# Optimization experiments

Measured on AMD Instinct MI355X. Metric: run time of the kernel, lower is better.

The kernel has to match this reference:

```python
import jax, jax.numpy as jnp
import numpy as np

B, T, C, H = 8, 2048, 1024, 128


def setup_inputs() -> dict:
    key = jax.random.key(0)
    k1, k2, k3, k4 = jax.random.split(key, 4)
    x = jax.random.normal(k1, (B, T, C), dtype=jnp.float32)
    # torch nn.Linear(n_embed, head_size, bias=False) weights, stored as [C, H] for x @ W
    scale = 1.0 / np.sqrt(C)
    Wk = jax.random.normal(k2, (C, H), dtype=jnp.float32) * scale
    Wq = jax.random.normal(k3, (C, H), dtype=jnp.float32) * scale
    Wv = jax.random.normal(k4, (C, H), dtype=jnp.float32) * scale
    return {"x": x, "Wk": Wk, "Wq": Wq, "Wv": Wv}


def reference(x, Wk, Wq, Wv):
    # Faithful translation of Head.forward (dropout = identity in eval mode).
    Bx, Tx, Cx = x.shape
    k = x @ Wk  # [B,T,H]
    q = x @ Wq  # [B,T,H]
    v = x @ Wv  # [B,T,H]
    # NOTE: original scales by C**-0.5 (n_embed), not head_size**-0.5.
    scores = jnp.einsum('bth,bsh->bts', q, k) * (Cx ** -0.5)  # [B,T,T]
    causal = jnp.tril(jnp.ones((Tx, Tx), dtype=bool))  # tril buffer
    scores = jnp.where(causal, scores, -jnp.inf)
    weights = jax.nn.softmax(scores, axis=-1)
    out = jnp.einsum('bts,bsh->bth', weights, v)  # [B,T,H]
    return out
```

## Files before the change

kernel.cpp:

```cpp
#include <hip/hip_runtime.h>
#include <type_traits>

#define Bn 8
#define Tn 2048
#define Cn 1024
#define Hn 128
#define Mn (Bn*Tn)

typedef __attribute__((ext_vector_type(4))) float f32x4;
typedef __attribute__((ext_vector_type(2))) float f32x2;
typedef __attribute__((ext_vector_type(16))) float f32x16;
typedef __attribute__((ext_vector_type(8))) short s16x8;
typedef __attribute__((ext_vector_type(4))) int i32x4;
typedef __attribute__((ext_vector_type(2))) int i32x2;
typedef unsigned int u32;

__device__ __forceinline__ unsigned short f2bf(float f) {
  union { float f; unsigned u; } v; v.f = f;
  unsigned r = v.u + 0x7FFFu + ((v.u >> 16) & 1u);
  return (unsigned short)(r >> 16);
}

__device__ __forceinline__ float bf2f(unsigned s) {
  return __builtin_bit_cast(float, s << 16);
}

__device__ __forceinline__ unsigned cvtpk(float lo, float hi) {
  unsigned r;
  asm("v_cvt_pk_bf16_f32 %0, %1, %2" : "=v"(r) : "v"(lo), "v"(hi));
  return r;
}

__device__ __forceinline__ i32x2 swap32(int a, int b) {
#if __has_builtin(__builtin_amdgcn_permlane32_swap)
  return __builtin_amdgcn_permlane32_swap(a, b, false, false);
#else
  int ax = __shfl_xor(a, 32), bx = __shfl_xor(b, 32);
  i32x2 r;
  r[0] = (threadIdx.x & 32) ? bx : a;
  r[1] = (threadIdx.x & 32) ? b : ax;
  return r;
#endif
}

__device__ __forceinline__ void gl_lds16(const void* g, void* l) {
  __builtin_amdgcn_global_load_lds((const __attribute__((address_space(1))) u32*)g,
                                   (__attribute__((address_space(3))) u32*)l, 16, 0, 0);
}

__global__ __launch_bounds__(256) void prep_wt(const float* __restrict__ Wq,
                                               const float* __restrict__ Wk,
                                               const float* __restrict__ Wv,
                                               unsigned short* __restrict__ Wt) {
  __shared__ float tile[64][33];
  const int w = blockIdx.z;
  const float* W = (w == 0) ? Wq : (w == 1) ? Wk : Wv;
  const float scale = (w == 0) ? 0.03125f : 1.0f;
  const int c0 = blockIdx.x * 64, h0 = blockIdx.y * 32;
  const int tid = threadIdx.x;
  const int hl = tid & 31, cg = tid >> 5;
#pragma unroll
  for (int i = 0; i < 8; i++) {
    int cl = cg * 8 + i;
    tile[cl][hl] = W[(c0 + cl) * Hn + h0 + hl];
  }
  __syncthreads();
  const int cl2 = tid & 63, hg = tid >> 6;
#pragma unroll
  for (int i = 0; i < 8; i++) {
    int hl2 = hg * 8 + i;
    Wt[(size_t)(w * Hn + h0 + hl2) * Cn + c0 + cl2] = f2bf(tile[cl2][hl2] * scale);
  }
}

__global__ __launch_bounds__(512, 1) void proj_fused(const float* __restrict__ x,
                                                     const unsigned short* __restrict__ Wt,
                                                     unsigned short* __restrict__ qkv) {
  __shared__ __align__(16) unsigned short Abuf[2][64 * 64];
  __shared__ __align__(16) unsigned short Bbuf[2][384 * 64];
  const int tid = threadIdx.x;
  const int lane = tid & 63, wv = tid >> 6;
  const int wm = wv >> 2, wn = wv & 3;
  const int l31 = lane & 31, hi = lane >> 5;
  const int bm = blockIdx.x * 64;
  const int phase = (blockIdx.x >> 3) & 15;

  const int ar = tid >> 3;
  const int as = tid & 7;

  f32x16 acc[3];
#pragma unroll
  for (int i = 0; i < 3; i++)
#pragma unroll
    for (int r = 0; r < 16; r++) acc[i][r] = 0.f;

  auto slice = [&](int u) { return ((u + phase) & 15) * 64; };

  auto stageB = [&](int buf, int kk) {
#pragma unroll
    for (int i = 0; i < 6; i++) {
      int r0 = wv * 48 + i * 8;
      int n = r0 + (lane >> 3);
      const unsigned short* src = Wt + (size_t)n * Cn + kk + (((lane & 7) ^ (n & 7)) << 3);
      gl_lds16(src, &Bbuf[buf][r0 * 64]);
    }
  };
  auto loadA = [&](int kk, float4& v0, float4& v1) {
    const float* g = x + (size_t)(bm + ar) * Cn + kk + as * 8;
    v0 = *(const float4*)g;
    v1 = *(const float4*)(g + 4);
  };
  auto writeA = [&](int buf, float4 v0, float4 v1) {
    i32x4 w = {(int)cvtpk(v0.x, v0.y), (int)cvtpk(v0.z, v0.w),
               (int)cvtpk(v1.x, v1.y), (int)cvtpk(v1.z, v1.w)};
    *(i32x4*)&Abuf[buf][ar * 64 + ((as ^ (ar & 7)) << 3)] = w;
  };

  {
    float4 a0, a1;
    loadA(slice(0), a0, a1);
    stageB(0, slice(0));
    writeA(0, a0, a1);
  }

  const int arow = wm * 32 + l31;

  auto body = [&](int u, auto PC) {
    constexpr int P = decltype(PC)::value;
    const bool more = (u < 15);
    float4 a0, a1;
    if (more) loadA(slice(u + 1), a0, a1);
    __builtin_amdgcn_s_barrier();
    if (more) {
      stageB(P ^ 1, slice(u + 1));
      asm volatile("s_waitcnt vmcnt(8) lgkmcnt(0)" ::: "memory");
    } else {
      asm volatile("s_waitcnt vmcnt(0) lgkmcnt(0)" ::: "memory");
    }
    __builtin_amdgcn_s_barrier();
    __builtin_amdgcn_sched_barrier(0);
    s16x8 aF[4];
#pragma unroll
    for (int ks = 0; ks < 4; ks++)
      aF[ks] = *(const s16x8*)&Abuf[P][arow * 64 + (((ks * 2 + hi) ^ (arow & 7)) << 3)];
    __builtin_amdgcn_s_setprio(1);
#pragma unroll
    for (int ks = 0; ks < 4; ks++)
#pragma unroll
      for (int ni = 0; ni < 3; ni++) {
        int brow = wn * 96 + ni * 32 + l31;
        s16x8 bF = *(const s16x8*)&Bbuf[P][brow * 64 + (((ks * 2 + hi) ^ (brow & 7)) << 3)];
        acc[ni] = __builtin_amdgcn_mfma_f32_32x32x16_bf16(aF[ks], bF, acc[ni], 0, 0, 0);
      }
    __builtin_amdgcn_s_setprio(0);
    if (more) writeA(P ^ 1, a0, a1);
  };

  for (int u = 0; u < 16; u += 2) {
    body(u, std::integral_constant<int, 0>{});
    body(u + 1, std::integral_constant<int, 1>{});
  }

#pragma unroll
  for (int ni = 0; ni < 3; ni++) {
    const int cb = wn * 3 + ni;
    if (cb < 8) {
      const int w = cb >> 2;
      const int h = (cb & 3) * 32 + l31;
      unsigned short* o = qkv + (size_t)w * ((size_t)Mn * Hn);
#pragma unroll
      for (int r = 0; r < 16; r++) {
        int m = bm + wm * 32 + (r & 3) + 8 * (r >> 2) + 4 * hi;
        o[(size_t)m * Hn + h] = f2bf(acc[ni][r]);
      }
    } else {
      const int h = (cb - 8) * 32 + l31;
      const int bb = bm >> 11;
      const int tl0 = (bm & 2047) + wm * 32;
      unsigned short* vt = qkv + (size_t)2 * Mn * Hn + (size_t)bb * (Hn * Tn) + (size_t)h * Tn;
#pragma unroll
      for (int r = 0; r < 16; r++)
        vt[tl0 + (r & 3) + 8 * (r >> 2) + 4 * hi] = f2bf(acc[ni][r]);
    }
  }
}

__global__ __launch_bounds__(256, 2) void attn_fwd(const unsigned short* __restrict__ qkv,
                                                   unsigned short* __restrict__ o_part,
                                                   float* __restrict__ ml,
                                                   int sshift) {
  __shared__ __align__(16) unsigned short Kl[2][64 * 128];
  __shared__ __align__(16) unsigned short Vl[2][128 * 64];

  const int bid = blockIdx.x;
  const int b = bid & 7;
  const int r = bid >> 3;
  const int jj = r & 15;
  const int sp = r >> 4;
  const int S = 1 << sshift;
  const int j = (S > 1 && sp >= (S >> 1)) ? (15 - jj) : jj;
  const int s = sp;

  const int tid = threadIdx.x;
  const int lane = tid & 63, wv = tid >> 6;
  const int l31 = lane & 31, hi = lane >> 5;

  const unsigned short* qb  = qkv + (size_t)b * (Tn * Hn);
  const unsigned short* kb  = qkv + (size_t)(Mn * Hn) + (size_t)b * (Tn * Hn);
  const unsigned short* vtb = qkv + (size_t)2 * (Mn * Hn) + (size_t)b * (Hn * Tn);

  const int qrow0 = j * 128 + wv * 32;
  const int qg = qrow0 + l31;

  const int ntt = (j + 1) * 2;
  const int tlo = (s * ntt) >> sshift;
  const int thi = ((s + 1) * ntt) >> sshift;

  f32x16 oT[4];
#pragma unroll
  for (int i = 0; i < 4; i++)
#pragma unroll
    for (int q = 0; q < 16; q++) oT[i][q] = 0.f;
  float m_ = -1e30f, l_ = 0.f;

  auto stage = [&](int buf, int tile) {
    const int kvb0 = tile * 64;
#pragma unroll
    for (int i = 0; i < 4; i++) {
      int r0 = wv * 16 + i * 4;
      int row = r0 + (lane >> 4);
      int ch = lane & 15;
      const unsigned short* src = kb + (size_t)(kvb0 + row) * Hn + ((ch ^ (row & 7)) << 3);
      gl_lds16(src, &Kl[buf][r0 * 128]);
    }
#pragma unroll
    for (int i = 0; i < 4; i++) {
      int r0 = wv * 32 + i * 8;
      int row = r0 + (lane >> 3);
      int ch = lane & 7;
      const unsigned short* src = vtb + (size_t)row * Tn + kvb0 + ((ch ^ (row & 7)) << 3);
      gl_lds16(src, &Vl[buf][r0 * 64]);
    }
  };

  if (tlo < thi) {
    s16x8 qB[8];
#pragma unroll
    for (int hs = 0; hs < 8; hs++)
      qB[hs] = *(const s16x8*)(qb + (size_t)qg * Hn + hs * 16 + hi * 8);

    stage(0, tlo);
    asm volatile("s_waitcnt vmcnt(0)");
    __syncthreads();
    int buf = 0;

    for (int t = tlo; t < thi; t++) {
      if (t + 1 < thi) stage(buf ^ 1, t + 1);
      const int kvb = t * 64;
      if (kvb < qrow0 + 32) {
        const unsigned short* Kb = &Kl[buf][0];
        f32x16 sv0, sv1;
#pragma unroll
        for (int q = 0; q < 16; q++) { sv0[q] = 0.f; sv1[q] = 0.f; }
        __builtin_amdgcn_s_setprio(1);
        {
          const int row = l31;
#pragma unroll
          for (int hs = 0; hs < 8; hs++) {
            s16x8 kf = *(const s16x8*)&Kb[row * 128 + (((hs * 2 + hi) ^ (row & 7)) << 3)];
            sv0 = __builtin_amdgcn_mfma_f32_32x32x16_bf16(kf, qB[hs], sv0, 0, 0, 0);
          }
        }
        {
          const int row = 32 + l31;
#pragma unroll
          for (int hs = 0; hs < 8; hs++) {
            s16x8 kf = *(const s16x8*)&Kb[row * 128 + (((hs * 2 + hi) ^ (row & 7)) << 3)];
            sv1 = __builtin_amdgcn_mfma_f32_32x32x16_bf16(kf, qB[hs], sv1, 0, 0, 0);
          }
        }
        __builtin_amdgcn_s_setprio(0);
        if (kvb + 63 > qrow0) {
#pragma unroll
          for (int q = 0; q < 16; q++) {
            int kr = (q & 3) + 8 * (q >> 2) + 4 * hi;
            if (kvb + kr > qg) sv0[q] = -1e30f;
            if (kvb + 32 + kr > qg) sv1[q] = -1e30f;
          }
        }
        float om = sv0[0];
#pragma unroll
        for (int q = 1; q < 16; q++) om = fmaxf(om, sv0[q]);
#pragma unroll
        for (int q = 0; q < 16; q++) om = fmaxf(om, sv1[q]);
        i32x2 mx = swap32(__builtin_bit_cast(int, om), __builtin_bit_cast(int, om));
        float pm = __builtin_bit_cast(float, hi ? mx[0] : mx[1]);
        float tmax = fmaxf(om, pm);
        if (__any(tmax > m_ + 8.f)) {
          float mn = fmaxf(m_, tmax);
          float sc = __expf(m_ - mn);
          m_ = mn; l_ *= sc;
#pragma unroll
          for (int i = 0; i < 4; i++)
#pragma unroll
            for (int q = 0; q < 16; q++) oT[i][q] *= sc;
        }
        float osum = 0.f;
#pragma unroll
        for (int q = 0; q < 16; q++) { sv0[q] = __expf(sv0[q] - m_); osum += sv0[q]; }
#pragma unroll
        for (int q = 0; q < 16; q++) { sv1[q] = __expf(sv1[q] - m_); osum += sv1[q]; }
        i32x2 sx = swap32(__builtin_bit_cast(int, osum), __builtin_bit_cast(int, osum));
        float psum = __builtin_bit_cast(float, hi ? sx[0] : sx[1]);
        l_ += osum + psum;
        s16x8 pB[4];
        {
          unsigned PK[8];
#pragma unroll
          for (int n = 0; n < 8; n++) PK[n] = cvtpk(sv0[2 * n], sv0[2 * n + 1]);
          i32x2 e0 = swap32((int)PK[0], (int)PK[2]);
          i32x2 e1 = swap32((int)PK[1], (int)PK[3]);
          i32x2 e2 = swap32((int)PK[4], (int)PK[6]);
          i32x2 e3 = swap32((int)PK[5], (int)PK[7]);
          i32x4 w0 = {e0[0], e1[0], e0[1], e1[1]};
          i32x4 w1 = {e2[0], e3[0], e2[1], e3[1]};
          pB[0] = __builtin_bit_cast(s16x8, w0);
          pB[1] = __builtin_bit_cast(s16x8, w1);
        }
        {
          unsigned PK[8];
#pragma unroll
          for (int n = 0; n < 8; n++) PK[n] = cvtpk(sv1[2 * n], sv1[2 * n + 1]);
          i32x2 e0 = swap32((int)PK[0], (int)PK[2]);
          i32x2 e1 = swap32((int)PK[1], (int)PK[3]);
          i32x2 e2 = swap32((int)PK[4], (int)PK[6]);
          i32x2 e3 = swap32((int)PK[5], (int)PK[7]);
          i32x4 w0 = {e0[0], e1[0], e0[1], e1[1]};
          i32x4 w1 = {e2[0], e3[0], e2[1], e3[1]};
          pB[2] = __builtin_bit_cast(s16x8, w0);
          pB[3] = __builtin_bit_cast(s16x8, w1);
        }
        __builtin_amdgcn_s_setprio(1);
#pragma unroll
        for (int hsl = 0; hsl < 4; hsl++) {
          const int row = hsl * 32 + l31;
#pragma unroll
          for (int ks = 0; ks < 4; ks++) {
            s16x8 vf = *(const s16x8*)&Vl[buf][row * 64 + (((ks * 2 + hi) ^ (row & 7)) << 3)];
            oT[hsl] = __builtin_amdgcn_mfma_f32_32x32x16_bf16(vf, pB[ks], oT[hsl], 0, 0, 0);
          }
        }
        __builtin_amdgcn_s_setprio(0);
      }
      asm volatile("s_waitcnt vmcnt(0)");
      __syncthreads();
      buf ^= 1;
    }
  }

  unsigned short* orow = o_part + (size_t)s * ((size_t)Mn * Hn) + (size_t)(b * Tn + qg) * Hn;
#pragma unroll
  for (int hsl = 0; hsl < 4; hsl++)
#pragma unroll
    for (int g = 0; g < 4; g++) {
      unsigned p0 = cvtpk(oT[hsl][4 * g + 0], oT[hsl][4 * g + 1]);
      unsigned p1 = cvtpk(oT[hsl][4 * g + 2], oT[hsl][4 * g + 3]);
      i32x2 st = {(int)p0, (int)p1};
      *(i32x2*)(orow + hsl * 32 + g * 8 + hi * 4) = st;
    }
  if (lane < 32) {
    f32x2 w = {m_, l_};
    *(f32x2*)(ml + (size_t)s * (Mn * 2) + (size_t)(b * Tn + qg) * 2) = w;
  }
}

__global__ __launch_bounds__(256) void combine(const unsigned short* __restrict__ o_part,
                                               const float* __restrict__ ml,
                                               float* __restrict__ out, int S) {
  const int q = blockIdx.x * 4 + (threadIdx.x >> 6);
  const int p = threadIdx.x & 63;
  float M = -1e30f;
  for (int s = 0; s < S; s++) M = fmaxf(M, ml[(size_t)s * (Mn * 2) + q * 2]);
  float L = 0.f, a0 = 0.f, a1 = 0.f;
  for (int s = 0; s < S; s++) {
    float ms = ml[(size_t)s * (Mn * 2) + q * 2];
    float ls = ml[(size_t)s * (Mn * 2) + q * 2 + 1];
    float w = __expf(ms - M);
    L += ls * w;
    u32 v = *(const u32*)(o_part + (size_t)s * ((size_t)Mn * Hn) + (size_t)q * Hn + p * 2);
    a0 += bf2f(v & 0xffffu) * w;
    a1 += bf2f(v >> 16) * w;
  }
  float2 o = {a0 / L, a1 / L};
  *(float2*)(out + (size_t)q * Hn + p * 2) = o;
}

extern "C" void kernel_launch(void* const* d_in, const int* in_sizes, int n_in,
                              void* d_out, int out_size, void* d_ws, size_t ws_size,
                              hipStream_t stream) {
  const float* x  = (const float*)d_in[0];
  const float* Wk = (const float*)d_in[1];
  const float* Wq = (const float*)d_in[2];
  const float* Wv = (const float*)d_in[3];
  float* out = (float*)d_out;

  char* ws = (char*)d_ws;
  const size_t wt_b  = 786432;
  const size_t qkv_b = (size_t)3 * Mn * Hn * 2;
  const size_t base  = wt_b + qkv_b;
  const size_t per   = (size_t)Mn * Hn * 2 + (size_t)Mn * 8;
  int sshift = (ws_size >= base + 4 * per) ? 2 : (ws_size >= base + 2 * per) ? 1 : 0;
  const int S = 1 << sshift;

  unsigned short* Wt  = (unsigned short*)ws;
  unsigned short* qkv = (unsigned short*)(ws + wt_b);
  unsigned short* o_part = (unsigned short*)(ws + base);
  float* mlp = (float*)(ws + base + (size_t)S * Mn * Hn * 2);

  prep_wt<<<dim3(16, 4, 3), 256, 0, stream>>>(Wq, Wk, Wv, Wt);
  proj_fused<<<256, 512, 0, stream>>>(x, Wt, qkv);
  attn_fwd<<<128 * S, 256, 0, stream>>>(qkv, o_part, mlp, sshift);
  combine<<<Mn / 4, 256, 0, stream>>>(o_part, mlp, out, S);
}
```

Before: 63.73 us.

## Pre-convert x to bf16 in a separate pass and stage A via direct-to-LDS loads

Adds a standalone kernel that converts the fp32 input x to bf16 in workspace. The projection GEMM then stages its A tiles with global_load_lds instead of register loads plus in-kernel conversion, and the setprio hints are removed. The aim is to take the conversion and register round-trip out of the GEMM pipeline. The cost is an extra full pass over x: a 64MB read and a 32MB write plus a 32MB re-read, where the old code read x only once. Workspace use grows, which may lower the split factor S chosen for attention.

```diff
diff --git a/kernel.cpp b/kernel.cpp
--- a/kernel.cpp
+++ b/kernel.cpp
@@ -46,6 +46,19 @@
 __device__ __forceinline__ void gl_lds16(const void* g, void* l) {
   __builtin_amdgcn_global_load_lds((const __attribute__((address_space(1))) u32*)g,
                                    (__attribute__((address_space(3))) u32*)l, 16, 0, 0);
+}
+
+__global__ __launch_bounds__(256) void cvt_x(const float* __restrict__ x,
+                                             unsigned short* __restrict__ xb) {
+  const size_t total = (size_t)Mn * Cn;
+  const size_t stride = (size_t)gridDim.x * 256 * 8;
+  for (size_t i = ((size_t)blockIdx.x * 256 + threadIdx.x) * 8; i < total; i += stride) {
+    float4 v0 = *(const float4*)(x + i);
+    float4 v1 = *(const float4*)(x + i + 4);
+    i32x4 w = {(int)cvtpk(v0.x, v0.y), (int)cvtpk(v0.z, v0.w),
+               (int)cvtpk(v1.x, v1.y), (int)cvtpk(v1.z, v1.w)};
+    *(i32x4*)(xb + i) = w;
+  }
 }
 
 __global__ __launch_bounds__(256) void prep_wt(const float* __restrict__ Wq,
@@ -73,7 +86,7 @@
   }
 }
 
-__global__ __launch_bounds__(512, 1) void proj_fused(const float* __restrict__ x,
+__global__ __launch_bounds__(512, 1) void proj_fused(const unsigned short* __restrict__ xb,
                                                      const unsigned short* __restrict__ Wt,
                                                      unsigned short* __restrict__ qkv) {
   __shared__ __align__(16) unsigned short Abuf[2][64 * 64];
@@ -85,9 +98,6 @@
   const int bm = blockIdx.x * 64;
   const int phase = (blockIdx.x >> 3) & 15;
 
-  const int ar = tid >> 3;
-  const int as = tid & 7;
-
   f32x16 acc[3];
 #pragma unroll
   for (int i = 0; i < 3; i++)
@@ -96,6 +106,12 @@
 
   auto slice = [&](int u) { return ((u + phase) & 15) * 64; };
 
+  auto stageA = [&](int buf, int kk) {
+    int row = wv * 8 + (lane >> 3);
+    int ch = lane & 7;
+    const unsigned short* src = xb + (size_t)(bm + row) * Cn + kk + ((ch ^ (row & 7)) << 3);
+    gl_lds16(src, &Abuf[buf][(wv * 8) * 64]);
+  };
   auto stageB = [&](int buf, int kk) {
 #pragma unroll
     for (int i = 0; i < 6; i++) {
@@ -105,37 +121,22 @@
       gl_lds16(src, &Bbuf[buf][r0 * 64]);
     }
   };
-  auto loadA = [&](int kk, float4& v0, float4& v1) {
-    const float* g = x + (size_t)(bm + ar) * Cn + kk + as * 8;
-    v0 = *(const float4*)g;
-    v1 = *(const float4*)(g + 4);
-  };
-  auto writeA = [&](int buf, float4 v0, float4 v1) {
-    i32x4 w = {(int)cvtpk(v0.x, v0.y), (int)cvtpk(v0.z, v0.w),
-               (int)cvtpk(v1.x, v1.y), (int)cvtpk(v1.z, v1.w)};
-    *(i32x4*)&Abuf[buf][ar * 64 + ((as ^ (ar & 7)) << 3)] = w;
-  };
-
-  {
-    float4 a0, a1;
-    loadA(slice(0), a0, a1);
-    stageB(0, slice(0));
-    writeA(0, a0, a1);
-  }
+
+  stageA(0, slice(0));
+  stageB(0, slice(0));
 
   const int arow = wm * 32 + l31;
 
   auto body = [&](int u, auto PC) {
     constexpr int P = decltype(PC)::value;
     const bool more = (u < 15);
-    float4 a0, a1;
-    if (more) loadA(slice(u + 1), a0, a1);
     __builtin_amdgcn_s_barrier();
     if (more) {
+      stageA(P ^ 1, slice(u + 1));
       stageB(P ^ 1, slice(u + 1));
-      asm volatile("s_waitcnt vmcnt(8) lgkmcnt(0)" ::: "memory");
+      asm volatile("s_waitcnt vmcnt(7)" ::: "memory");
     } else {
-      asm volatile("s_waitcnt vmcnt(0) lgkmcnt(0)" ::: "memory");
+      asm volatile("s_waitcnt vmcnt(0)" ::: "memory");
     }
     __builtin_amdgcn_s_barrier();
     __builtin_amdgcn_sched_barrier(0);
@@ -143,7 +144,6 @@
 #pragma unroll
     for (int ks = 0; ks < 4; ks++)
       aF[ks] = *(const s16x8*)&Abuf[P][arow * 64 + (((ks * 2 + hi) ^ (arow & 7)) << 3)];
-    __builtin_amdgcn_s_setprio(1);
 #pragma unroll
     for (int ks = 0; ks < 4; ks++)
 #pragma unroll
@@ -152,8 +152,6 @@
         s16x8 bF = *(const s16x8*)&Bbuf[P][brow * 64 + (((ks * 2 + hi) ^ (brow & 7)) << 3)];
         acc[ni] = __builtin_amdgcn_mfma_f32_32x32x16_bf16(aF[ks], bF, acc[ni], 0, 0, 0);
       }
-    __builtin_amdgcn_s_setprio(0);
-    if (more) writeA(P ^ 1, a0, a1);
   };
 
   for (int u = 0; u < 16; u += 2) {
@@ -407,18 +405,21 @@
   char* ws = (char*)d_ws;
   const size_t wt_b  = 786432;
   const size_t qkv_b = (size_t)3 * Mn * Hn * 2;
-  const size_t base  = wt_b + qkv_b;
+  const size_t xb_b  = (size_t)Mn * Cn * 2;
+  const size_t base  = wt_b + qkv_b + xb_b;
   const size_t per   = (size_t)Mn * Hn * 2 + (size_t)Mn * 8;
   int sshift = (ws_size >= base + 4 * per) ? 2 : (ws_size >= base + 2 * per) ? 1 : 0;
   const int S = 1 << sshift;
 
   unsigned short* Wt  = (unsigned short*)ws;
   unsigned short* qkv = (unsigned short*)(ws + wt_b);
+  unsigned short* xb  = (unsigned short*)(ws + wt_b + qkv_b);
   unsigned short* o_part = (unsigned short*)(ws + base);
   float* mlp = (float*)(ws + base + (size_t)S * Mn * Hn * 2);
 
+  cvt_x<<<2048, 256, 0, stream>>>(x, xb);
   prep_wt<<<dim3(16, 4, 3), 256, 0, stream>>>(Wq, Wk, Wv, Wt);
-  proj_fused<<<256, 512, 0, stream>>>(x, Wt, qkv);
+  proj_fused<<<256, 512, 0, stream>>>(xb, Wt, qkv);
   attn_fwd<<<128 * S, 256, 0, stream>>>(qkv, o_part, mlp, sshift);
   combine<<<Mn / 4, 256, 0, stream>>>(o_part, mlp, out, S);
 }
```

New measurement: 76.10 us. +19.4%, slower.

## Split fused QKV projection into per-weight blocks with smaller tiles

Applied to the files above, without the earlier changes.

The fused projection, where one 512-thread block computed Q, K and V for 64 rows, is replaced by a 3D grid. Each of three 256-thread blocks per row tile handles one weight matrix, with a 128-wide B tile and up to 3 blocks per CU. This raises block count and occupancy to hide latency, but each x tile is now read and converted three times instead of once. It also moves the A global loads after the first barrier and drops the setprio hints.

```diff
diff --git a/kernel.cpp b/kernel.cpp
--- a/kernel.cpp
+++ b/kernel.cpp
@@ -73,24 +73,25 @@
   }
 }
 
-__global__ __launch_bounds__(512, 1) void proj_fused(const float* __restrict__ x,
-                                                     const unsigned short* __restrict__ Wt,
-                                                     unsigned short* __restrict__ qkv) {
+__global__ __launch_bounds__(256, 3) void proj3(const float* __restrict__ x,
+                                                const unsigned short* __restrict__ Wt,
+                                                unsigned short* __restrict__ qkv) {
   __shared__ __align__(16) unsigned short Abuf[2][64 * 64];
-  __shared__ __align__(16) unsigned short Bbuf[2][384 * 64];
+  __shared__ __align__(16) unsigned short Bbuf[2][128 * 64];
   const int tid = threadIdx.x;
   const int lane = tid & 63, wv = tid >> 6;
-  const int wm = wv >> 2, wn = wv & 3;
+  const int wm = wv >> 1, wn = wv & 1;
   const int l31 = lane & 31, hi = lane >> 5;
   const int bm = blockIdx.x * 64;
+  const int w = blockIdx.y;
   const int phase = (blockIdx.x >> 3) & 15;
 
-  const int ar = tid >> 3;
-  const int as = tid & 7;
-
-  f32x16 acc[3];
-#pragma unroll
-  for (int i = 0; i < 3; i++)
+  const int ar = tid >> 2;
+  const int ac = (tid & 3) * 2;
+
+  f32x16 acc[2];
+#pragma unroll
+  for (int i = 0; i < 2; i++)
 #pragma unroll
     for (int r = 0; r < 16; r++) acc[i][r] = 0.f;
 
@@ -98,29 +99,35 @@
 
   auto stageB = [&](int buf, int kk) {
 #pragma unroll
-    for (int i = 0; i < 6; i++) {
-      int r0 = wv * 48 + i * 8;
-      int n = r0 + (lane >> 3);
-      const unsigned short* src = Wt + (size_t)n * Cn + kk + (((lane & 7) ^ (n & 7)) << 3);
+    for (int i = 0; i < 4; i++) {
+      int r0 = wv * 32 + i * 8;
+      int row = r0 + (lane >> 3);
+      const unsigned short* src = Wt + (size_t)(w * Hn + row) * Cn + kk +
+                                  (((lane & 7) ^ (row & 7)) << 3);
       gl_lds16(src, &Bbuf[buf][r0 * 64]);
     }
   };
-  auto loadA = [&](int kk, float4& v0, float4& v1) {
-    const float* g = x + (size_t)(bm + ar) * Cn + kk + as * 8;
-    v0 = *(const float4*)g;
-    v1 = *(const float4*)(g + 4);
+  auto loadA = [&](int kk, float4& R0, float4& R1, float4& R2, float4& R3) {
+    const float* g = x + (size_t)(bm + ar) * Cn + kk + ac * 8;
+    R0 = *(const float4*)g;
+    R1 = *(const float4*)(g + 4);
+    R2 = *(const float4*)(g + 8);
+    R3 = *(const float4*)(g + 12);
   };
-  auto writeA = [&](int buf, float4 v0, float4 v1) {
-    i32x4 w = {(int)cvtpk(v0.x, v0.y), (int)cvtpk(v0.z, v0.w),
-               (int)cvtpk(v1.x, v1.y), (int)cvtpk(v1.z, v1.w)};
-    *(i32x4*)&Abuf[buf][ar * 64 + ((as ^ (ar & 7)) << 3)] = w;
+  auto writeA = [&](int buf, float4 R0, float4 R1, float4 R2, float4 R3) {
+    i32x4 w0 = {(int)cvtpk(R0.x, R0.y), (int)cvtpk(R0.z, R0.w),
+                (int)cvtpk(R1.x, R1.y), (int)cvtpk(R1.z, R1.w)};
+    i32x4 w1 = {(int)cvtpk(R2.x, R2.y), (int)cvtpk(R2.z, R2.w),
+                (int)cvtpk(R3.x, R3.y), (int)cvtpk(R3.z, R3.w)};
+    *(i32x4*)&Abuf[buf][ar * 64 + ((ac ^ (ar & 7)) << 3)] = w0;
+    *(i32x4*)&Abuf[buf][ar * 64 + (((ac + 1) ^ (ar & 7)) << 3)] = w1;
   };
 
   {
-    float4 a0, a1;
-    loadA(slice(0), a0, a1);
+    float4 R0, R1, R2, R3;
+    loadA(slice(0), R0, R1, R2, R3);
     stageB(0, slice(0));
-    writeA(0, a0, a1);
+    writeA(0, R0, R1, R2, R3);
   }
 
   const int arow = wm * 32 + l31;
@@ -128,10 +135,10 @@
   auto body = [&](int u, auto PC) {
     constexpr int P = decltype(PC)::value;
     const bool more = (u < 15);
-    float4 a0, a1;
-    if (more) loadA(slice(u + 1), a0, a1);
     __builtin_amdgcn_s_barrier();
+    float4 R0, R1, R2, R3;
     if (more) {
+      loadA(slice(u + 1), R0, R1, R2, R3);
       stageB(P ^ 1, slice(u + 1));
       asm volatile("s_waitcnt vmcnt(8) lgkmcnt(0)" ::: "memory");
     } else {
@@ -143,17 +150,15 @@
 #pragma unroll
     for (int ks = 0; ks < 4; ks++)
       aF[ks] = *(const s16x8*)&Abuf[P][arow * 64 + (((ks * 2 + hi) ^ (arow & 7)) << 3)];
-    __builtin_amdgcn_s_setprio(1);
 #pragma unroll
     for (int ks = 0; ks < 4; ks++)
 #pragma unroll
-      for (int ni = 0; ni < 3; ni++) {
-        int brow = wn * 96 + ni * 32 + l31;
+      for (int ni = 0; ni < 2; ni++) {
+        int brow = wn * 64 + ni * 32 + l31;
         s16x8 bF = *(const s16x8*)&Bbuf[P][brow * 64 + (((ks * 2 + hi) ^ (brow & 7)) << 3)];
         acc[ni] = __builtin_amdgcn_mfma_f32_32x32x16_bf16(aF[ks], bF, acc[ni], 0, 0, 0);
       }
-    __builtin_amdgcn_s_setprio(0);
-    if (more) writeA(P ^ 1, a0, a1);
+    if (more) writeA(P ^ 1, R0, R1, R2, R3);
   };
 
   for (int u = 0; u < 16; u += 2) {
@@ -162,11 +167,10 @@
   }
 
 #pragma unroll
-  for (int ni = 0; ni < 3; ni++) {
-    const int cb = wn * 3 + ni;
-    if (cb < 8) {
-      const int w = cb >> 2;
-      const int h = (cb & 3) * 32 + l31;
+  for (int ni = 0; ni < 2; ni++) {
+    const int cb = wn * 2 + ni;
+    const int h = cb * 32 + l31;
+    if (w < 2) {
       unsigned short* o = qkv + (size_t)w * ((size_t)Mn * Hn);
 #pragma unroll
       for (int r = 0; r < 16; r++) {
@@ -174,7 +178,6 @@
         o[(size_t)m * Hn + h] = f2bf(acc[ni][r]);
       }
     } else {
-      const int h = (cb - 8) * 32 + l31;
       const int bb = bm >> 11;
       const int tl0 = (bm & 2047) + wm * 32;
       unsigned short* vt = qkv + (size_t)2 * Mn * Hn + (size_t)bb * (Hn * Tn) + (size_t)h * Tn;
@@ -418,7 +421,7 @@
   float* mlp = (float*)(ws + base + (size_t)S * Mn * Hn * 2);
 
   prep_wt<<<dim3(16, 4, 3), 256, 0, stream>>>(Wq, Wk, Wv, Wt);
-  proj_fused<<<256, 512, 0, stream>>>(x, Wt, qkv);
+  proj3<<<dim3(256, 3), 256, 0, stream>>>(x, Wt, qkv);
   attn_fwd<<<128 * S, 256, 0, stream>>>(qkv, o_part, mlp, sshift);
   combine<<<Mn / 4, 256, 0, stream>>>(o_part, mlp, out, S);
 }
```

After: 66.04 us. 3.6% more time.
